# Performance work log

Hardware: AMD Instinct MI355X
Metric: run time of the kernel (lower is better)

Reference implementation:

```python
import jax, jax.numpy as jnp
import numpy as np

B, T, H = 8, 2048, 512


def _minimaxn(x):
    # global min-max normalization (NetTransform.minimaxn)
    mx = jnp.max(x)
    mn = jnp.min(x)
    return (x - mn) / (mx - mn)


def _fb(e):
    # NetTransform.fb, mode='batch', vectorized over the batch.
    # e: (B, 1, T) -> (B, 1, T, T)
    # Result: out[b,0,i,j] = prod(e[b,0,j:i]) for i>j, 1 on diag, 0 above diag.
    x = e[:, 0]                                   # (B, T)
    Bsz, Tsz = x.shape
    X = jnp.broadcast_to(x[:, :, None], (Bsz, Tsz, Tsz))  # xs = x.unsqueeze(-1).repeat(1,1,T)
    tril1 = jnp.tril(jnp.ones((Tsz, Tsz), x.dtype))
    m_f = jnp.triu(jnp.ones((Tsz, Tsz), x.dtype), 1)
    A = X * tril1 + m_f                           # tril(x) + m_f
    C = jnp.cumprod(A, axis=1)                    # cumprod along dim -2
    S = jnp.concatenate([jnp.ones((Bsz, 1, Tsz), x.dtype), C[:, :-1]], axis=1) - m_f
    return S[:, None]                             # (B, 1, T, T)


def _clustering(energy_t):
    # NetTransform.clustering (tnum == 1), vectorized over batch.
    # energy_t: (B, 1, T) -> bool mask (B, 1, T) with top-num_neg of (1-energy) set True
    x = 1.0 - energy_t[:, 0]                      # (B, T)
    num_neg = x.sum(-1).astype(jnp.int32)         # int() truncation; x >= 0 so == floor
    ranks = jnp.argsort(jnp.argsort(-x, axis=-1), axis=-1)  # rank 0 = largest
    m = ranks < num_neg[:, None]
    return m[:, None]                             # (B, 1, T)


def setup_inputs() -> dict:
    key = jax.random.key(0)
    k1, k2, k3 = jax.random.split(key, 3)
    e = jax.random.uniform(k1, (B, 1, T), dtype=jnp.float32)
    h = jax.random.normal(k2, (B, 1, T, H), dtype=jnp.float32)
    ilens = jnp.concatenate([
        jnp.array([T], dtype=jnp.int32),
        jax.random.randint(k3, (B - 1,), T // 2, T + 1).astype(jnp.int32),
    ])
    return {"e": e, "h": h, "ilens": ilens}


def reference(e, h, ilens):
    sg = jax.lax.stop_gradient
    # energy_t = minimaxn(flows['e']).detach()
    energy_t = sg(_minimaxn(e))                   # (B, 1, T)
    # clustering mask (computed in forward; unused when cutting_gauge == 0)
    _ = _clustering(energy_t)
    # energy_t_cumprod = fb(energy_t)  (under no_grad)
    K = sg(_fb(energy_t))                         # (B, 1, T, T)
    # h_agg = (K @ h) / K.sum(-1, keepdim), then transpose(-2, -1)
    h_agg = jnp.einsum('bnts,bnsh->bnth', K, h) / K.sum(-1, keepdims=True)
    h_agg = jnp.swapaxes(h_agg, -2, -1)           # (B, 1, H, T)
    # kernel = (h @ h_agg.detach() + h.detach() @ h_agg) / 2 / sqrt(H)
    kernel = (jnp.matmul(h, sg(h_agg)) + jnp.matmul(sg(h), h_agg)) / 2.0 / np.sqrt(H).astype(np.float32)
    return kernel                                 # (B, 1, T, T)
```

## Files before the change

### kernel.cpp

```cpp
#include <hip/hip_runtime.h>
#include <hip/hip_bf16.h>
#include <stdint.h>

#define B_DIM 8
#define T_DIM 2048
#define H_DIM 512
#define NC 32
#define LCH 64
#define BM 128
#define BN 128
#define BK 32

typedef float floatx4 __attribute__((ext_vector_type(4)));
typedef __bf16 bf16x8 __attribute__((ext_vector_type(8)));

__global__ __launch_bounds__(1024) void minmax_kernel(const float* __restrict__ e,
                                                      float* __restrict__ stats) {
    const float4* e4 = (const float4*)e;
    int tid = threadIdx.x;
    float mn = 1e30f, mx = -1e30f;
    #pragma unroll
    for (int i = 0; i < 4; ++i) {
        float4 v = e4[tid + i * 1024];
        mn = fminf(mn, fminf(fminf(v.x, v.y), fminf(v.z, v.w)));
        mx = fmaxf(mx, fmaxf(fmaxf(v.x, v.y), fmaxf(v.z, v.w)));
    }
    for (int off = 32; off > 0; off >>= 1) {
        mn = fminf(mn, __shfl_down(mn, off, 64));
        mx = fmaxf(mx, __shfl_down(mx, off, 64));
    }
    __shared__ float smn[16], smx[16];
    int wid = tid >> 6;
    if ((tid & 63) == 0) { smn[wid] = mn; smx[wid] = mx; }
    __syncthreads();
    if (tid == 0) {
        mn = smn[0]; mx = smx[0];
        #pragma unroll
        for (int w = 1; w < 16; ++w) { mn = fminf(mn, smn[w]); mx = fmaxf(mx, smx[w]); }
        stats[0] = mn;
        stats[1] = 1.0f / (mx - mn);
    }
}

__global__ __launch_bounds__(512) void chunk_sum_kernel(
        const float* __restrict__ e, const float* __restrict__ h,
        const float* __restrict__ stats,
        __hip_bfloat16* __restrict__ h_bf,
        float* __restrict__ Lend, float* __restrict__ PPend, float* __restrict__ LDend) {
    const int b = blockIdx.x, c = blockIdx.y, hd = threadIdx.x;
    const int t0 = c * LCH;
    const float mn = stats[0], sc = stats[1];
    const float* eb = e + b * T_DIM;
    const float* hp = h + ((size_t)b * T_DIM + t0) * H_DIM + hd;
    __hip_bfloat16* hbp = h_bf + ((size_t)b * T_DIM + t0) * H_DIM + hd;

    float lv = 0.0f, ldv = 0.0f, pp = 1.0f;
    #pragma unroll 8
    for (int i = 0; i < LCH; ++i) {
        int t = t0 + i;
        float a = (t == 0) ? 0.0f : (eb[t - 1] - mn) * sc;
        float hv = hp[(size_t)i * H_DIM];
        lv = fmaf(a, lv, hv);
        ldv = fmaf(a, ldv, 1.0f);
        pp *= a;
        hbp[(size_t)i * H_DIM] = __float2bfloat16(hv);
    }
    Lend[((size_t)b * NC + c) * H_DIM + hd] = lv;
    if (hd == 0) { PPend[b * NC + c] = pp; LDend[b * NC + c] = ldv; }
}

__global__ __launch_bounds__(512) void carry_kernel(
        const float* __restrict__ Lend, const float* __restrict__ PPend,
        const float* __restrict__ LDend,
        float* __restrict__ S, float* __restrict__ SD) {
    const int b = blockIdx.x, hd = threadIdx.x;
    float s = 0.0f, sd = 0.0f;
    #pragma unroll
    for (int c = 0; c < NC; ++c) {
        S[((size_t)b * NC + c) * H_DIM + hd] = s;
        if (hd == 0) SD[b * NC + c] = sd;
        float pe = PPend[b * NC + c];
        s  = fmaf(pe, s,  Lend[((size_t)b * NC + c) * H_DIM + hd]);
        sd = fmaf(pe, sd, LDend[b * NC + c]);
    }
}

__global__ __launch_bounds__(512) void rescan_kernel(
        const float* __restrict__ e, const __hip_bfloat16* __restrict__ h_bf,
        const float* __restrict__ stats,
        const float* __restrict__ S, const float* __restrict__ SD,
        __hip_bfloat16* __restrict__ hagg_bf) {
    const int b = blockIdx.x, c = blockIdx.y, hd = threadIdx.x;
    const int t0 = c * LCH;
    const float mn = stats[0], sc = stats[1];
    const float* eb = e + b * T_DIM;
    const __hip_bfloat16* hbp = h_bf + ((size_t)b * T_DIM + t0) * H_DIM + hd;
    __hip_bfloat16* hop = hagg_bf + ((size_t)b * T_DIM + t0) * H_DIM + hd;

    float s  = S[((size_t)b * NC + c) * H_DIM + hd];
    float sd = SD[b * NC + c];
    #pragma unroll 8
    for (int i = 0; i < LCH; ++i) {
        int t = t0 + i;
        float a = (t == 0) ? 0.0f : (eb[t - 1] - mn) * sc;
        float hv = __bfloat162float(hbp[(size_t)i * H_DIM]);
        s  = fmaf(a, s, hv);
        sd = fmaf(a, sd, 1.0f);
        hop[(size_t)i * H_DIM] = __float2bfloat16(s / sd);
    }
}

__device__ __forceinline__ void async16(const void* g, void* l) {
    __builtin_amdgcn_global_load_lds(
        (__attribute__((address_space(1))) void*)g,
        (__attribute__((address_space(3))) void*)l,
        16, 0, 0);
}

__global__ __launch_bounds__(256) void gemm_kernel(
        const __hip_bfloat16* __restrict__ Abf,
        const __hip_bfloat16* __restrict__ Bbf,
        float* __restrict__ C) {
    __shared__ __align__(16) __hip_bfloat16 As[BM * BK];
    __shared__ __align__(16) __hip_bfloat16 Bs[BN * BK];
    const int b = blockIdx.z;
    const int tm = blockIdx.x * BM;
    const int sn = blockIdx.y * BN;
    const int tid = threadIdx.x;
    const int lane = tid & 63;
    const int wave = tid >> 6;
    const int wm = (wave >> 1) * 64;
    const int wn = (wave & 1) * 64;
    const int l16 = lane & 15;
    const int quad = lane >> 4;

    const __hip_bfloat16* Ag = Abf + ((size_t)b * T_DIM + tm + (tid >> 2)) * H_DIM + (tid & 3) * 8;
    const __hip_bfloat16* Bg = Bbf + ((size_t)b * T_DIM + sn + (tid >> 2)) * H_DIM + (tid & 3) * 8;
    char* AsB = (char*)As;
    char* BsB = (char*)Bs;

    floatx4 zero = {0.0f, 0.0f, 0.0f, 0.0f};
    floatx4 acc[4][4];
    #pragma unroll
    for (int i = 0; i < 4; ++i)
        #pragma unroll
        for (int j = 0; j < 4; ++j) acc[i][j] = zero;

    for (int kk = 0; kk < H_DIM; kk += BK) {
        __syncthreads();
        async16(Ag + kk,                AsB + tid * 16);
        async16(Ag + kk + 64 * H_DIM,   AsB + 4096 + tid * 16);
        async16(Bg + kk,                BsB + tid * 16);
        async16(Bg + kk + 64 * H_DIM,   BsB + 4096 + tid * 16);
        asm volatile("s_waitcnt vmcnt(0)" ::: "memory");
        __syncthreads();

        bf16x8 af[4], bfv[4];
        #pragma unroll
        for (int i = 0; i < 4; ++i) {
            af[i]  = *reinterpret_cast<const bf16x8*>(AsB + ((wm + i * 16 + l16) * BK + quad * 8) * 2);
            bfv[i] = *reinterpret_cast<const bf16x8*>(BsB + ((wn + i * 16 + l16) * BK + quad * 8) * 2);
        }
        #pragma unroll
        for (int i = 0; i < 4; ++i)
            #pragma unroll
            for (int j = 0; j < 4; ++j)
                acc[i][j] = __builtin_amdgcn_mfma_f32_16x16x32_bf16(af[i], bfv[j], acc[i][j], 0, 0, 0);
    }

    const float scale = 0.04419417382415922f;
    float* Cp = C + (size_t)b * T_DIM * T_DIM;
    #pragma unroll
    for (int i = 0; i < 4; ++i) {
        int row0 = tm + wm + i * 16 + quad * 4;
        #pragma unroll
        for (int j = 0; j < 4; ++j) {
            int col = sn + wn + j * 16 + l16;
            #pragma unroll
            for (int r = 0; r < 4; ++r)
                Cp[(size_t)(row0 + r) * T_DIM + col] = acc[i][j][r] * scale;
        }
    }
}

extern "C" void kernel_launch(void* const* d_in, const int* in_sizes, int n_in,
                              void* d_out, int out_size, void* d_ws, size_t ws_size,
                              hipStream_t stream) {
    const float* e = (const float*)d_in[0];
    const float* h = (const float*)d_in[1];
    float* out = (float*)d_out;

    char* ws = (char*)d_ws;
    float* stats            = (float*)ws;
    __hip_bfloat16* h_bf    = (__hip_bfloat16*)(ws + 256);
    __hip_bfloat16* hagg_bf = (__hip_bfloat16*)(ws + 256 + (16u << 20));
    char* p = ws + 256 + (32u << 20);
    float* Lend  = (float*)p;                    p += (size_t)B_DIM * NC * H_DIM * 4;
    float* PPend = (float*)p;                    p += B_DIM * NC * 4;
    float* LDend = (float*)p;                    p += B_DIM * NC * 4;
    float* S     = (float*)p;                    p += (size_t)B_DIM * NC * H_DIM * 4;
    float* SD    = (float*)p;

    minmax_kernel<<<1, 1024, 0, stream>>>(e, stats);
    chunk_sum_kernel<<<dim3(B_DIM, NC), 512, 0, stream>>>(e, h, stats, h_bf, Lend, PPend, LDend);
    carry_kernel<<<B_DIM, 512, 0, stream>>>(Lend, PPend, LDend, S, SD);
    rescan_kernel<<<dim3(B_DIM, NC), 512, 0, stream>>>(e, h_bf, stats, S, SD, hagg_bf);
    gemm_kernel<<<dim3(T_DIM / BM, T_DIM / BN, B_DIM), 256, 0, stream>>>(h_bf, hagg_bf, out);
}
```

Measured before the change: 243.7 us.

## Fuse chunked scan stages with flag-based carry and enlarge swizzled GEMM K-tile

Merges the chunk-sum, carry and rescan kernels into one kernel. Each block publishes its chunk summary through a release flag, then spin-waits on its predecessors' flags and recomputes its carry from their summaries, which removes two launches and the separate carry pass. It also doubles the GEMM K tile to 64 and XOR-swizzles the LDS layout to avoid bank conflicts, halving the number of barrier-synchronised load steps. The cost is spin-waiting, which relies on all 256 scan blocks being co-resident (likely on this GPU), and a carry loop whose length grows with the chunk index.

```diff
diff --git a/kernel.cpp b/kernel.cpp
--- a/kernel.cpp
+++ b/kernel.cpp
@@ -9,15 +9,17 @@
 #define LCH 64
 #define BM 128
 #define BN 128
-#define BK 32
+#define BK 64
 
 typedef float floatx4 __attribute__((ext_vector_type(4)));
 typedef __bf16 bf16x8 __attribute__((ext_vector_type(8)));
 
 __global__ __launch_bounds__(1024) void minmax_kernel(const float* __restrict__ e,
-                                                      float* __restrict__ stats) {
+                                                      float* __restrict__ stats,
+                                                      int* __restrict__ flags) {
     const float4* e4 = (const float4*)e;
     int tid = threadIdx.x;
+    if (tid < B_DIM * NC) flags[tid] = 0;
     float mn = 1e30f, mx = -1e30f;
     #pragma unroll
     for (int i = 0; i < 4; ++i) {
@@ -42,17 +44,20 @@
     }
 }
 
-__global__ __launch_bounds__(512) void chunk_sum_kernel(
+__global__ __launch_bounds__(512) void fused_scan_kernel(
         const float* __restrict__ e, const float* __restrict__ h,
         const float* __restrict__ stats,
         __hip_bfloat16* __restrict__ h_bf,
-        float* __restrict__ Lend, float* __restrict__ PPend, float* __restrict__ LDend) {
+        float* __restrict__ Lend, float* __restrict__ PPend, float* __restrict__ LDend,
+        __hip_bfloat16* __restrict__ hagg_bf,
+        int* __restrict__ flags) {
     const int b = blockIdx.x, c = blockIdx.y, hd = threadIdx.x;
     const int t0 = c * LCH;
     const float mn = stats[0], sc = stats[1];
     const float* eb = e + b * T_DIM;
     const float* hp = h + ((size_t)b * T_DIM + t0) * H_DIM + hd;
     __hip_bfloat16* hbp = h_bf + ((size_t)b * T_DIM + t0) * H_DIM + hd;
+    __hip_bfloat16* hop = hagg_bf + ((size_t)b * T_DIM + t0) * H_DIM + hd;
 
     float lv = 0.0f, ldv = 0.0f, pp = 1.0f;
     #pragma unroll 8
@@ -67,46 +72,34 @@
     }
     Lend[((size_t)b * NC + c) * H_DIM + hd] = lv;
     if (hd == 0) { PPend[b * NC + c] = pp; LDend[b * NC + c] = ldv; }
-}
-
-__global__ __launch_bounds__(512) void carry_kernel(
-        const float* __restrict__ Lend, const float* __restrict__ PPend,
-        const float* __restrict__ LDend,
-        float* __restrict__ S, float* __restrict__ SD) {
-    const int b = blockIdx.x, hd = threadIdx.x;
-    float s = 0.0f, sd = 0.0f;
-    #pragma unroll
-    for (int c = 0; c < NC; ++c) {
-        S[((size_t)b * NC + c) * H_DIM + hd] = s;
-        if (hd == 0) SD[b * NC + c] = sd;
-        float pe = PPend[b * NC + c];
-        s  = fmaf(pe, s,  Lend[((size_t)b * NC + c) * H_DIM + hd]);
-        sd = fmaf(pe, sd, LDend[b * NC + c]);
-    }
-}
-
-__global__ __launch_bounds__(512) void rescan_kernel(
-        const float* __restrict__ e, const __hip_bfloat16* __restrict__ h_bf,
-        const float* __restrict__ stats,
-        const float* __restrict__ S, const float* __restrict__ SD,
-        __hip_bfloat16* __restrict__ hagg_bf) {
-    const int b = blockIdx.x, c = blockIdx.y, hd = threadIdx.x;
-    const int t0 = c * LCH;
-    const float mn = stats[0], sc = stats[1];
-    const float* eb = e + b * T_DIM;
-    const __hip_bfloat16* hbp = h_bf + ((size_t)b * T_DIM + t0) * H_DIM + hd;
-    __hip_bfloat16* hop = hagg_bf + ((size_t)b * T_DIM + t0) * H_DIM + hd;
-
-    float s  = S[((size_t)b * NC + c) * H_DIM + hd];
-    float sd = SD[b * NC + c];
+    __syncthreads();
+    if (hd == 0) {
+        __threadfence();
+        __hip_atomic_store(&flags[b * NC + c], 1, __ATOMIC_RELEASE, __HIP_MEMORY_SCOPE_AGENT);
+    }
+
+    if (hd < c) {
+        while (__hip_atomic_load(&flags[b * NC + hd], __ATOMIC_ACQUIRE,
+                                 __HIP_MEMORY_SCOPE_AGENT) == 0) {
+            __builtin_amdgcn_s_sleep(2);
+        }
+    }
+    __syncthreads();
+    float s = 0.0f, sdv = 0.0f;
+    for (int cp = 0; cp < c; ++cp) {
+        float pe = PPend[b * NC + cp];
+        s   = fmaf(pe, s,   Lend[((size_t)b * NC + cp) * H_DIM + hd]);
+        sdv = fmaf(pe, sdv, LDend[b * NC + cp]);
+    }
+
     #pragma unroll 8
     for (int i = 0; i < LCH; ++i) {
         int t = t0 + i;
         float a = (t == 0) ? 0.0f : (eb[t - 1] - mn) * sc;
         float hv = __bfloat162float(hbp[(size_t)i * H_DIM]);
-        s  = fmaf(a, s, hv);
-        sd = fmaf(a, sd, 1.0f);
-        hop[(size_t)i * H_DIM] = __float2bfloat16(s / sd);
+        s   = fmaf(a, s, hv);
+        sdv = fmaf(a, sdv, 1.0f);
+        hop[(size_t)i * H_DIM] = __float2bfloat16(s / sdv);
     }
 }
 
@@ -134,8 +127,10 @@
     const int l16 = lane & 15;
     const int quad = lane >> 4;
 
-    const __hip_bfloat16* Ag = Abf + ((size_t)b * T_DIM + tm + (tid >> 2)) * H_DIM + (tid & 3) * 8;
-    const __hip_bfloat16* Bg = Bbf + ((size_t)b * T_DIM + sn + (tid >> 2)) * H_DIM + (tid & 3) * 8;
+    const int srow = tid >> 3;
+    const int sgran = (tid & 7) ^ (srow & 7);
+    const __hip_bfloat16* Ag = Abf + ((size_t)b * T_DIM + tm + srow) * H_DIM + sgran * 8;
+    const __hip_bfloat16* Bg = Bbf + ((size_t)b * T_DIM + sn + srow) * H_DIM + sgran * 8;
     char* AsB = (char*)As;
     char* BsB = (char*)Bs;
 
@@ -148,24 +143,32 @@
 
     for (int kk = 0; kk < H_DIM; kk += BK) {
         __syncthreads();
-        async16(Ag + kk,                AsB + tid * 16);
-        async16(Ag + kk + 64 * H_DIM,   AsB + 4096 + tid * 16);
-        async16(Bg + kk,                BsB + tid * 16);
-        async16(Bg + kk + 64 * H_DIM,   BsB + 4096 + tid * 16);
+        #pragma unroll
+        for (int q = 0; q < 4; ++q) {
+            async16(Ag + (size_t)q * 32 * H_DIM + kk, AsB + q * 4096 + tid * 16);
+            async16(Bg + (size_t)q * 32 * H_DIM + kk, BsB + q * 4096 + tid * 16);
+        }
         asm volatile("s_waitcnt vmcnt(0)" ::: "memory");
         __syncthreads();
 
-        bf16x8 af[4], bfv[4];
-        #pragma unroll
-        for (int i = 0; i < 4; ++i) {
-            af[i]  = *reinterpret_cast<const bf16x8*>(AsB + ((wm + i * 16 + l16) * BK + quad * 8) * 2);
-            bfv[i] = *reinterpret_cast<const bf16x8*>(BsB + ((wn + i * 16 + l16) * BK + quad * 8) * 2);
-        }
-        #pragma unroll
-        for (int i = 0; i < 4; ++i)
+        bf16x8 af[2][4], bfv[2][4];
+        #pragma unroll
+        for (int ku = 0; ku < 2; ++ku)
             #pragma unroll
-            for (int j = 0; j < 4; ++j)
-                acc[i][j] = __builtin_amdgcn_mfma_f32_16x16x32_bf16(af[i], bfv[j], acc[i][j], 0, 0, 0);
+            for (int i = 0; i < 4; ++i) {
+                int ra = wm + i * 16 + l16;
+                int rb = wn + i * 16 + l16;
+                int ga = (ku * 4 + quad) ^ (l16 & 7);
+                af[ku][i]  = *reinterpret_cast<const bf16x8*>(AsB + ra * 128 + ga * 16);
+                bfv[ku][i] = *reinterpret_cast<const bf16x8*>(BsB + rb * 128 + ga * 16);
+            }
+        #pragma unroll
+        for (int ku = 0; ku < 2; ++ku)
+            #pragma unroll
+            for (int i = 0; i < 4; ++i)
+                #pragma unroll
+                for (int j = 0; j < 4; ++j)
+                    acc[i][j] = __builtin_amdgcn_mfma_f32_16x16x32_bf16(af[ku][i], bfv[ku][j], acc[i][j], 0, 0, 0);
     }
 
     const float scale = 0.04419417382415922f;
@@ -192,18 +195,16 @@
 
     char* ws = (char*)d_ws;
     float* stats            = (float*)ws;
-    __hip_bfloat16* h_bf    = (__hip_bfloat16*)(ws + 256);
-    __hip_bfloat16* hagg_bf = (__hip_bfloat16*)(ws + 256 + (16u << 20));
-    char* p = ws + 256 + (32u << 20);
-    float* Lend  = (float*)p;                    p += (size_t)B_DIM * NC * H_DIM * 4;
-    float* PPend = (float*)p;                    p += B_DIM * NC * 4;
-    float* LDend = (float*)p;                    p += B_DIM * NC * 4;
-    float* S     = (float*)p;                    p += (size_t)B_DIM * NC * H_DIM * 4;
-    float* SD    = (float*)p;
-
-    minmax_kernel<<<1, 1024, 0, stream>>>(e, stats);
-    chunk_sum_kernel<<<dim3(B_DIM, NC), 512, 0, stream>>>(e, h, stats, h_bf, Lend, PPend, LDend);
-    carry_kernel<<<B_DIM, 512, 0, stream>>>(Lend, PPend, LDend, S, SD);
-    rescan_kernel<<<dim3(B_DIM, NC), 512, 0, stream>>>(e, h_bf, stats, S, SD, hagg_bf);
+    int* flags              = (int*)(ws + 256);
+    __hip_bfloat16* h_bf    = (__hip_bfloat16*)(ws + 4096);
+    __hip_bfloat16* hagg_bf = (__hip_bfloat16*)(ws + 4096 + (16u << 20));
+    char* p = ws + 4096 + (32u << 20);
+    float* Lend  = (float*)p;   p += (size_t)B_DIM * NC * H_DIM * 4;
+    float* PPend = (float*)p;   p += B_DIM * NC * 4;
+    float* LDend = (float*)p;
+
+    minmax_kernel<<<1, 1024, 0, stream>>>(e, stats, flags);
+    fused_scan_kernel<<<dim3(B_DIM, NC), 512, 0, stream>>>(
+        e, h, stats, h_bf, Lend, PPend, LDend, hagg_bf, flags);
     gemm_kernel<<<dim3(T_DIM / BM, T_DIM / BN, B_DIM), 256, 0, stream>>>(h_bf, hagg_bf, out);
 }
```

Result: slower. 251.2 us (+3.1%).
